# Optimization experiments

Measured on AMD Instinct MI355X. Metric: run time of the kernel, lower is better.

Reference implementation:

```python
import jax, jax.numpy as jnp
import numpy as np

B, LP, LQ, H = 16, 2048, 2048, 1024

def setup_inputs() -> dict:
    key = jax.random.key(0)
    k1, k2, k3 = jax.random.split(key, 3)
    proj_p = jax.random.normal(k1, (B, LP, H), dtype=jnp.float32)
    proj_q = jax.random.normal(k2, (B, LQ, H), dtype=jnp.float32)
    # nn.Linear(hidden_size, hidden_size): W stored as [out, in], y = x @ W.T + b
    W = jax.random.normal(k3, (H, H), dtype=jnp.float32) * (1.0 / np.sqrt(H))
    b = jnp.zeros((H,), dtype=jnp.float32)
    return {"proj_p": proj_p, "proj_q": proj_q, "W": W, "b": b}

def reference(proj_p, proj_q, W, b):
    # trans_q = Linear(proj_q)
    trans_q = jnp.einsum('bqh,oh->bqo', proj_q, W) + b            # [B,LQ,H]
    # UNscaled attention scores: proj_p @ trans_q^T
    att_weights = jnp.einsum('bph,bqh->bpq', proj_p, trans_q)     # [B,LP,LQ]
    att_norm = jax.nn.softmax(att_weights, axis=-1)
    att_vec = jnp.einsum('bpq,bqh->bph', att_norm, proj_q)        # [B,LP,H]
    # same linear weight reused, then ReLU
    out = jax.nn.relu(jnp.einsum('bph,oh->bpo', att_vec, W) + b)
    return out
```

## Files before the change

kernel.cpp:

```cpp
#include <hip/hip_runtime.h>

typedef _Float16 f16;
typedef _Float16 f16x8 __attribute__((ext_vector_type(8)));
typedef _Float16 f16x4 __attribute__((ext_vector_type(4)));
typedef float    f32x16 __attribute__((ext_vector_type(16)));

#define GLDS(gp, lp) __builtin_amdgcn_global_load_lds( \
    (const __attribute__((address_space(1))) void*)(gp), \
    (__attribute__((address_space(3))) void*)(lp), 16, 0, 0)

template<typename OUT_T, bool BIAS, bool RELU>
__global__ __launch_bounds__(512, 2)
void gemm_bt2(const f16* __restrict__ A, const f16* __restrict__ Bm,
              OUT_T* __restrict__ C, const float* __restrict__ bias,
              int M, int N, int K, long sA, long sB, long sC)
{
    constexpr int TSZ = 256 * 64;
    __shared__ alignas(16) f16 As[2 * TSZ];
    __shared__ alignas(16) f16 Bs[2 * TSZ];

    int bx = blockIdx.x, by = blockIdx.y;
    {
        const int gx = gridDim.x;
        const int l = by * gx + bx;
        const int W = gx * 8;
        const int ygrp = l / W;
        const int rem = l - ygrp * W;
        bx = rem >> 3;
        by = ygrp * 8 + (rem & 7);
    }
    const int z = blockIdx.z;
    A  += (long)z * sA;
    Bm += (long)z * sB;
    C  += (long)z * sC;

    const int tid  = threadIdx.x;
    const int wid  = tid >> 6;
    const int lane = tid & 63;
    const int lr = lane & 31;
    const int lh = lane >> 5;
    const int m0 = by * 256;
    const int n0 = bx * 256;
    const int wm = (wid >> 2) * 128;
    const int wn = (wid & 3) * 64;

    const int sr = tid >> 3;
    const int sg = ((tid & 7) ^ (sr & 7)) * 8;
    const f16* agS = A  + (long)(m0 + sr) * K + sg;
    const f16* bgS = Bm + (long)(n0 + sr) * K + sg;
    f16* aD = As + wid * (8 * 64);
    f16* bD = Bs + wid * (8 * 64);

    const int s7  = lr & 7;
    const int xs0 = ((0 + lh) ^ s7) * 8;
    const int xs1 = ((2 + lh) ^ s7) * 8;
    const int xs2 = ((4 + lh) ^ s7) * 8;
    const int xs3 = ((6 + lh) ^ s7) * 8;
    const f16* aR = As + (wm + lr) * 64;
    const f16* bR = Bs + (wn + lr) * 64;

    f32x16 acc[4][2];
#pragma unroll
    for (int mi = 0; mi < 4; ++mi)
#pragma unroll
        for (int ni = 0; ni < 2; ++ni)
#pragma unroll
            for (int r = 0; r < 16; ++r) acc[mi][ni][r] = 0.f;

    f16x8 b00, b01, b02, b03, b10, b11, b12, b13;

    const int NT = K >> 6;

#define GAc(buf, R0, kt) GLDS(agS + (long)(R0) * K + (kt), aD + (buf) * TSZ + (R0) * 64)
#define GBc(buf, R0, kt) GLDS(bgS + (long)(R0) * K + (kt), bD + (buf) * TSZ + (R0) * 64)

    GBc(0,   0, 0);  GBc(0,  64, 0);  GBc(0, 128, 0);  GBc(0, 192, 0);
    GAc(0,   0, 0);  GAc(0,  64, 0);  GAc(0, 128, 0);  GAc(0, 192, 0);
    GBc(1,   0, 64); GBc(1,  64, 64); GBc(1, 128, 64); GBc(1, 192, 64);
    GAc(1,   0, 64); GAc(1, 128, 64);
    asm volatile("s_waitcnt vmcnt(6)" ::: "memory");
    __builtin_amdgcn_s_barrier();

#define MFMA8(mi) \
    acc[mi][0] = __builtin_amdgcn_mfma_f32_32x32x16_f16(af0, b00, acc[mi][0], 0, 0, 0); \
    acc[mi][1] = __builtin_amdgcn_mfma_f32_32x32x16_f16(af0, b10, acc[mi][1], 0, 0, 0); \
    acc[mi][0] = __builtin_amdgcn_mfma_f32_32x32x16_f16(af1, b01, acc[mi][0], 0, 0, 0); \
    acc[mi][1] = __builtin_amdgcn_mfma_f32_32x32x16_f16(af1, b11, acc[mi][1], 0, 0, 0); \
    acc[mi][0] = __builtin_amdgcn_mfma_f32_32x32x16_f16(af2, b02, acc[mi][0], 0, 0, 0); \
    acc[mi][1] = __builtin_amdgcn_mfma_f32_32x32x16_f16(af2, b12, acc[mi][1], 0, 0, 0); \
    acc[mi][0] = __builtin_amdgcn_mfma_f32_32x32x16_f16(af3, b03, acc[mi][0], 0, 0, 0); \
    acc[mi][1] = __builtin_amdgcn_mfma_f32_32x32x16_f16(af3, b13, acc[mi][1], 0, 0, 0);

#define PH(buf, mi, VW, ...) { \
    if ((mi) == 0) { \
        b00 = *(const f16x8*)(bR + (buf) * TSZ + xs0); \
        b01 = *(const f16x8*)(bR + (buf) * TSZ + xs1); \
        b02 = *(const f16x8*)(bR + (buf) * TSZ + xs2); \
        b03 = *(const f16x8*)(bR + (buf) * TSZ + xs3); \
        b10 = *(const f16x8*)(bR + (buf) * TSZ + 2048 + xs0); \
        b11 = *(const f16x8*)(bR + (buf) * TSZ + 2048 + xs1); \
        b12 = *(const f16x8*)(bR + (buf) * TSZ + 2048 + xs2); \
        b13 = *(const f16x8*)(bR + (buf) * TSZ + 2048 + xs3); \
    } \
    f16x8 af0 = *(const f16x8*)(aR + (buf) * TSZ + (mi) * 2048 + xs0); \
    f16x8 af1 = *(const f16x8*)(aR + (buf) * TSZ + (mi) * 2048 + xs1); \
    f16x8 af2 = *(const f16x8*)(aR + (buf) * TSZ + (mi) * 2048 + xs2); \
    f16x8 af3 = *(const f16x8*)(aR + (buf) * TSZ + (mi) * 2048 + xs3); \
    __VA_ARGS__ \
    __builtin_amdgcn_s_barrier(); \
    asm volatile("s_waitcnt lgkmcnt(0)" ::: "memory"); \
    __builtin_amdgcn_s_setprio(1); \
    MFMA8(mi) \
    __builtin_amdgcn_s_setprio(0); \
    if (VW) { asm volatile("s_waitcnt vmcnt(6)" ::: "memory"); } \
    __builtin_amdgcn_s_barrier(); \
}

    for (int i = 0; i < NT / 2; ++i) {
        const long k1 = (long)(2 * i + 1) << 6;
        const long kA = (2 * i + 2 < NT) ? ((long)(2 * i + 2) << 6) : 0;
        const long kB = (2 * i + 3 < NT) ? ((long)(2 * i + 3) << 6) : 0;
        PH(0, 0, 0, GAc(1,  64, k1); GAc(1, 192, k1);)
        PH(0, 1, 0, GBc(0,   0, kA); GBc(0,  64, kA);)
        PH(0, 2, 0, GBc(0, 128, kA); GBc(0, 192, kA);)
        PH(0, 3, 1, GAc(0,   0, kA); GAc(0, 128, kA);)
        PH(1, 0, 0, GAc(0,  64, kA); GAc(0, 192, kA);)
        PH(1, 1, 0, GBc(1,   0, kB); GBc(1,  64, kB);)
        PH(1, 2, 0, GBc(1, 128, kB); GBc(1, 192, kB);)
        PH(1, 3, 1, GAc(1,   0, kB); GAc(1, 128, kB);)
    }

    asm volatile("s_waitcnt vmcnt(0)" ::: "memory");

#pragma unroll
    for (int ni = 0; ni < 2; ++ni) {
        const int gc = n0 + wn + ni * 32 + lr;
        const float bv = BIAS ? bias[gc] : 0.0f;
#pragma unroll
        for (int mi = 0; mi < 4; ++mi) {
#pragma unroll
            for (int r = 0; r < 16; ++r) {
                const int row = (r & 3) + 8 * (r >> 2) + 4 * lh;
                const int gr = m0 + wm + mi * 32 + row;
                float v = acc[mi][ni][r] + bv;
                if (RELU) v = fmaxf(v, 0.0f);
                C[(long)gr * N + gc] = (OUT_T)v;
            }
        }
    }
#undef PH
#undef MFMA8
#undef GAc
#undef GBc
}

template<typename OUT_T, bool BIAS, bool RELU>
__global__ __launch_bounds__(512, 2)
void gemm_bt3(const f16* __restrict__ A, const f16* __restrict__ Bm,
              OUT_T* __restrict__ C, const float* __restrict__ bias,
              int M, int N, int K, long sA, long sB, long sC)
{
    constexpr int TSA = 256 * 64;
    constexpr int TSB = 128 * 64;
    __shared__ alignas(16) f16 As[2 * TSA];
    __shared__ alignas(16) f16 Bs[2 * TSB];

    int bx = blockIdx.x, by = blockIdx.y;
    {
        const int gx = gridDim.x;
        const int l = by * gx + bx;
        const int W = gx * 8;
        const int ygrp = l / W;
        const int rem = l - ygrp * W;
        bx = rem >> 3;
        by = ygrp * 8 + (rem & 7);
    }
    const int z = blockIdx.z;
    A  += (long)z * sA;
    Bm += (long)z * sB;
    C  += (long)z * sC;

    const int tid  = threadIdx.x;
    const int wid  = tid >> 6;
    const int lane = tid & 63;
    const int lr = lane & 31;
    const int lh = lane >> 5;
    const int m0 = by * 256;
    const int n0 = bx * 128;
    const int wm = (wid >> 1) * 64;
    const int wn = (wid & 1) * 64;

    const int sr = tid >> 3;
    const int sg = ((tid & 7) ^ (sr & 7)) * 8;
    const f16* agS = A  + (long)(m0 + sr) * K + sg;
    const f16* bgS = Bm + (long)(n0 + sr) * K + sg;
    f16* aD = As + wid * (8 * 64);
    f16* bD = Bs + wid * (8 * 64);

    const int s7  = lr & 7;
    const int xs0 = ((0 + lh) ^ s7) * 8;
    const int xs1 = ((2 + lh) ^ s7) * 8;
    const int xs2 = ((4 + lh) ^ s7) * 8;
    const int xs3 = ((6 + lh) ^ s7) * 8;
    const f16* aR = As + (wm + lr) * 64;
    const f16* bR = Bs + (wn + lr) * 64;

    f32x16 acc[2][2];
#pragma unroll
    for (int mi = 0; mi < 2; ++mi)
#pragma unroll
        for (int ni = 0; ni < 2; ++ni)
#pragma unroll
            for (int r = 0; r < 16; ++r) acc[mi][ni][r] = 0.f;

    f16x8 b00, b01, b02, b03, b10, b11, b12, b13;

    const int NT = K >> 6;

#define GA3(buf, R0, kt) GLDS(agS + (long)(R0) * K + (kt), aD + (buf) * TSA + (R0) * 64)
#define GB3(buf, R0, kt) GLDS(bgS + (long)(R0) * K + (kt), bD + (buf) * TSB + (R0) * 64)

    GB3(0,   0, 0);  GB3(0,  64, 0);
    GA3(0,   0, 0);  GA3(0,  64, 0);  GA3(0, 128, 0);  GA3(0, 192, 0);
    GB3(1,   0, 64); GB3(1,  64, 64);
    asm volatile("s_waitcnt vmcnt(2)" ::: "memory");
    __builtin_amdgcn_s_barrier();

#define MFMA8_3(mi) \
    acc[mi][0] = __builtin_amdgcn_mfma_f32_32x32x16_f16(af0, b00, acc[mi][0], 0, 0, 0); \
    acc[mi][1] = __builtin_amdgcn_mfma_f32_32x32x16_f16(af0, b10, acc[mi][1], 0, 0, 0); \
    acc[mi][0] = __builtin_amdgcn_mfma_f32_32x32x16_f16(af1, b01, acc[mi][0], 0, 0, 0); \
    acc[mi][1] = __builtin_amdgcn_mfma_f32_32x32x16_f16(af1, b11, acc[mi][1], 0, 0, 0); \
    acc[mi][0] = __builtin_amdgcn_mfma_f32_32x32x16_f16(af2, b02, acc[mi][0], 0, 0, 0); \
    acc[mi][1] = __builtin_amdgcn_mfma_f32_32x32x16_f16(af2, b12, acc[mi][1], 0, 0, 0); \
    acc[mi][0] = __builtin_amdgcn_mfma_f32_32x32x16_f16(af3, b03, acc[mi][0], 0, 0, 0); \
    acc[mi][1] = __builtin_amdgcn_mfma_f32_32x32x16_f16(af3, b13, acc[mi][1], 0, 0, 0);

#define PH3(buf, mi, VW, ...) { \
    if ((mi) == 0) { \
        b00 = *(const f16x8*)(bR + (buf) * TSB + xs0); \
        b01 = *(const f16x8*)(bR + (buf) * TSB + xs1); \
        b02 = *(const f16x8*)(bR + (buf) * TSB + xs2); \
        b03 = *(const f16x8*)(bR + (buf) * TSB + xs3); \
        b10 = *(const f16x8*)(bR + (buf) * TSB + 2048 + xs0); \
        b11 = *(const f16x8*)(bR + (buf) * TSB + 2048 + xs1); \
        b12 = *(const f16x8*)(bR + (buf) * TSB + 2048 + xs2); \
        b13 = *(const f16x8*)(bR + (buf) * TSB + 2048 + xs3); \
    } \
    f16x8 af0 = *(const f16x8*)(aR + (buf) * TSA + (mi) * 2048 + xs0); \
    f16x8 af1 = *(const f16x8*)(aR + (buf) * TSA + (mi) * 2048 + xs1); \
    f16x8 af2 = *(const f16x8*)(aR + (buf) * TSA + (mi) * 2048 + xs2); \
    f16x8 af3 = *(const f16x8*)(aR + (buf) * TSA + (mi) * 2048 + xs3); \
    __VA_ARGS__ \
    __builtin_amdgcn_s_barrier(); \
    asm volatile("s_waitcnt lgkmcnt(0)" ::: "memory"); \
    __builtin_amdgcn_s_setprio(1); \
    MFMA8_3(mi) \
    __builtin_amdgcn_s_setprio(0); \
    if (VW) { asm volatile("s_waitcnt vmcnt(2)" ::: "memory"); } \
    __builtin_amdgcn_s_barrier(); \
}

    for (int i = 0; i < NT / 2; ++i) {
        const long k1 = (long)(2 * i + 1) << 6;
        const long kA = (2 * i + 2 < NT) ? ((long)(2 * i + 2) << 6) : 0;
        const long kB = (2 * i + 3 < NT) ? ((long)(2 * i + 3) << 6) : 0;
        PH3(0, 0, 0, GA3(1,   0, k1); GA3(1,  64, k1); GA3(1, 128, k1); GA3(1, 192, k1);)
        PH3(0, 1, 1, GB3(0,   0, kA); GB3(0,  64, kA);)
        PH3(1, 0, 0, GA3(0,   0, kA); GA3(0,  64, kA); GA3(0, 128, kA); GA3(0, 192, kA);)
        PH3(1, 1, 1, GB3(1,   0, kB); GB3(1,  64, kB);)
    }

    asm volatile("s_waitcnt vmcnt(0)" ::: "memory");

#pragma unroll
    for (int ni = 0; ni < 2; ++ni) {
        const int gc = n0 + wn + ni * 32 + lr;
        const float bv = BIAS ? bias[gc] : 0.0f;
#pragma unroll
        for (int mi = 0; mi < 2; ++mi) {
#pragma unroll
            for (int r = 0; r < 16; ++r) {
                const int row = (r & 3) + 8 * (r >> 2) + 4 * lh;
                const int gr = m0 + wm + mi * 32 + row;
                float v = acc[mi][ni][r] + bv;
                if (RELU) v = fmaxf(v, 0.0f);
                C[(long)gr * N + gc] = (OUT_T)v;
            }
        }
    }
#undef PH3
#undef MFMA8_3
#undef GA3
#undef GB3
}

__global__ __launch_bounds__(256)
void cast_f32_f16(const float* __restrict__ X, f16* __restrict__ Y)
{
    const long i = ((long)blockIdx.x * 256 + threadIdx.x) * 8;
    float4 a = *(const float4*)(X + i);
    float4 b = *(const float4*)(X + i + 4);
    f16x8 h = {(f16)a.x, (f16)a.y, (f16)a.z, (f16)a.w,
               (f16)b.x, (f16)b.y, (f16)b.z, (f16)b.w};
    *(f16x8*)(Y + i) = h;
}

__global__ __launch_bounds__(256)
void cast_q_dual(const float* __restrict__ X, f16* __restrict__ Yrow,
                 f16* __restrict__ Ytr)
{
    __shared__ f16 t[64][72];
    const float* Xb = X + (long)blockIdx.z * (2048L * 1024);
    f16* Yrb = Yrow + (long)blockIdx.z * (2048L * 1024);
    f16* Ytb = Ytr  + (long)blockIdx.z * (1024L * 2048);
    const int r0 = blockIdx.y * 64;
    const int c0 = blockIdx.x * 64;
    const int tid = threadIdx.x;
    const int tr = tid >> 4;
    const int tc = (tid & 15) * 4;
#pragma unroll
    for (int rr = 0; rr < 64; rr += 16) {
        float4 v = *(const float4*)(Xb + (long)(r0 + tr + rr) * 1024 + c0 + tc);
        f16x4 h = {(f16)v.x, (f16)v.y, (f16)v.z, (f16)v.w};
        *(f16x4*)&t[tr + rr][tc] = h;
        *(f16x4*)(Yrb + (long)(r0 + tr + rr) * 1024 + c0 + tc) = h;
    }
    __syncthreads();
#pragma unroll
    for (int rr = 0; rr < 64; rr += 16) {
        const int orow = tr + rr;
        f16x4 o = {t[tc + 0][orow], t[tc + 1][orow], t[tc + 2][orow], t[tc + 3][orow]};
        *(f16x4*)(Ytb + (long)(c0 + orow) * 2048 + r0 + tc) = o;
    }
}

__global__ __launch_bounds__(256)
void softmax_p(const float* __restrict__ S, f16* __restrict__ P)
{
    const long row = blockIdx.x;
    const float* s = S + row * 2048;
    f16* p = P + row * 2048;
    const int tid = threadIdx.x;
    const int wid = tid >> 6, lane = tid & 63;

    float4 a = *(const float4*)(s + tid * 8);
    float4 b = *(const float4*)(s + tid * 8 + 4);
    float v[8] = {a.x, a.y, a.z, a.w, b.x, b.y, b.z, b.w};

    float m = v[0];
#pragma unroll
    for (int j = 1; j < 8; ++j) m = fmaxf(m, v[j]);
#pragma unroll
    for (int off = 32; off > 0; off >>= 1) m = fmaxf(m, __shfl_xor(m, off, 64));

    __shared__ float red[8];
    if (lane == 0) red[wid] = m;
    __syncthreads();
    m = fmaxf(fmaxf(red[0], red[1]), fmaxf(red[2], red[3]));

    float sum = 0.f;
#pragma unroll
    for (int j = 0; j < 8; ++j) { v[j] = __expf(v[j] - m); sum += v[j]; }
#pragma unroll
    for (int off = 32; off > 0; off >>= 1) sum += __shfl_xor(sum, off, 64);
    if (lane == 0) red[4 + wid] = sum;
    __syncthreads();
    sum = red[4] + red[5] + red[6] + red[7];

    const float inv = 1.0f / sum;
    f16x8 h = {(f16)(v[0] * inv), (f16)(v[1] * inv), (f16)(v[2] * inv), (f16)(v[3] * inv),
               (f16)(v[4] * inv), (f16)(v[5] * inv), (f16)(v[6] * inv), (f16)(v[7] * inv)};
    *(f16x8*)(p + tid * 8) = h;
}

extern "C" void kernel_launch(void* const* d_in, const int* in_sizes, int n_in,
                              void* d_out, int out_size, void* d_ws, size_t ws_size,
                              hipStream_t stream)
{
    const float* proj_p = (const float*)d_in[0];
    const float* proj_q = (const float*)d_in[1];
    const float* W      = (const float*)d_in[2];
    const float* bias   = (const float*)d_in[3];
    float* out = (float*)d_out;

    constexpr long Bc = 16, L = 2048, H = 1024, NB = 4;
    constexpr long nPQ = Bc * L * H;

    char* ws = (char*)d_ws;
    f16*   pB  = (f16*)(ws + 0L);
    f16*   qB  = (f16*)(ws + 67108864L);
    f16*   qBt = (f16*)(ws + 134217728L);
    f16*   tQ  = (f16*)(ws + 201326592L);
    f16*   aV  = (f16*)(ws + 268435456L);
    f16*   Wb  = (f16*)(ws + 335544320L);
    float* S   = (float*)(ws + 337641472L);
    f16*   P   = (f16*)(ws + 404750336L);

    cast_f32_f16<<<nPQ / (256 * 8), 256, 0, stream>>>(proj_p, pB);
    cast_f32_f16<<<(H * H) / (256 * 8), 256, 0, stream>>>(W, Wb);
    cast_q_dual<<<dim3(16, 32, 16), 256, 0, stream>>>(proj_q, qB, qBt);

    gemm_bt2<f16, true, false><<<dim3(H / 256, (Bc * L) / 256, 1), 512, 0, stream>>>(
        qB, Wb, tQ, bias, (int)(Bc * L), (int)H, (int)H, 0, 0, 0);

    for (int c = 0; c < 4; ++c) {
        const long boff = (long)c * NB * L * H;
        gemm_bt2<float, false, false><<<dim3(L / 256, L / 256, NB), 512, 0, stream>>>(
            pB + boff, tQ + boff, S, nullptr, (int)L, (int)L, (int)H,
            L * H, L * H, L * L);
        softmax_p<<<NB * L, 256, 0, stream>>>(S, P);
        gemm_bt3<f16, false, false><<<dim3(H / 128, L / 256, NB), 512, 0, stream>>>(
            P, qBt + (long)c * NB * H * L, aV + boff, nullptr, (int)L, (int)H, (int)L,
            L * L, H * L, L * H);
    }

    gemm_bt2<float, false, true><<<dim3(H / 256, (Bc * L) / 256, 1), 512, 0, stream>>>(
        aV, Wb, out, bias, (int)(Bc * L), (int)H, (int)H, 0, 0, 0);
}
```

Measured before the change: 968.3 us.

## Load B operand directly from global into registers, bypassing LDS

Both GEMM kernels now stop staging the B tile in shared memory. Each wave loads its own B fragments straight from global memory into registers, issuing one tile ahead, and the vmcnt waits are adjusted to match. This removes the LDS traffic, LDS capacity and barrier coupling for B, which could improve occupancy. In exchange, B data that several waves of a block share is fetched redundantly through L2/L1, and the global-load latency must be hidden by register prefetching, which raises register pressure.

```diff
diff --git a/kernel.cpp b/kernel.cpp
--- a/kernel.cpp
+++ b/kernel.cpp
@@ -17,7 +17,6 @@
 {
     constexpr int TSZ = 256 * 64;
     __shared__ alignas(16) f16 As[2 * TSZ];
-    __shared__ alignas(16) f16 Bs[2 * TSZ];
 
     int bx = blockIdx.x, by = blockIdx.y;
     {
@@ -46,10 +45,8 @@
 
     const int sr = tid >> 3;
     const int sg = ((tid & 7) ^ (sr & 7)) * 8;
-    const f16* agS = A  + (long)(m0 + sr) * K + sg;
-    const f16* bgS = Bm + (long)(n0 + sr) * K + sg;
+    const f16* agS = A + (long)(m0 + sr) * K + sg;
     f16* aD = As + wid * (8 * 64);
-    f16* bD = Bs + wid * (8 * 64);
 
     const int s7  = lr & 7;
     const int xs0 = ((0 + lh) ^ s7) * 8;
@@ -57,7 +54,9 @@
     const int xs2 = ((4 + lh) ^ s7) * 8;
     const int xs3 = ((6 + lh) ^ s7) * 8;
     const f16* aR = As + (wm + lr) * 64;
-    const f16* bR = Bs + (wn + lr) * 64;
+
+    const f16* bgl0 = Bm + (long)(n0 + wn + lr) * K + lh * 8;
+    const f16* bgl1 = bgl0 + (long)32 * K;
 
     f32x16 acc[4][2];
 #pragma unroll
@@ -67,41 +66,34 @@
 #pragma unroll
             for (int r = 0; r < 16; ++r) acc[mi][ni][r] = 0.f;
 
-    f16x8 b00, b01, b02, b03, b10, b11, b12, b13;
+    f16x8 bb0, bb1, bb2, bb3, bb4, bb5, bb6, bb7;
 
     const int NT = K >> 6;
 
 #define GAc(buf, R0, kt) GLDS(agS + (long)(R0) * K + (kt), aD + (buf) * TSZ + (R0) * 64)
-#define GBc(buf, R0, kt) GLDS(bgS + (long)(R0) * K + (kt), bD + (buf) * TSZ + (R0) * 64)
-
-    GBc(0,   0, 0);  GBc(0,  64, 0);  GBc(0, 128, 0);  GBc(0, 192, 0);
+#define BLD(kt) __builtin_amdgcn_sched_barrier(0); \
+    bb0 = *(const f16x8*)(bgl0 + (kt));      bb1 = *(const f16x8*)(bgl0 + (kt) + 16); \
+    bb2 = *(const f16x8*)(bgl0 + (kt) + 32); bb3 = *(const f16x8*)(bgl0 + (kt) + 48); \
+    bb4 = *(const f16x8*)(bgl1 + (kt));      bb5 = *(const f16x8*)(bgl1 + (kt) + 16); \
+    bb6 = *(const f16x8*)(bgl1 + (kt) + 32); bb7 = *(const f16x8*)(bgl1 + (kt) + 48);
+
+    BLD(0)
     GAc(0,   0, 0);  GAc(0,  64, 0);  GAc(0, 128, 0);  GAc(0, 192, 0);
-    GBc(1,   0, 64); GBc(1,  64, 64); GBc(1, 128, 64); GBc(1, 192, 64);
     GAc(1,   0, 64); GAc(1, 128, 64);
-    asm volatile("s_waitcnt vmcnt(6)" ::: "memory");
+    asm volatile("s_waitcnt vmcnt(2)" ::: "memory");
     __builtin_amdgcn_s_barrier();
 
 #define MFMA8(mi) \
-    acc[mi][0] = __builtin_amdgcn_mfma_f32_32x32x16_f16(af0, b00, acc[mi][0], 0, 0, 0); \
-    acc[mi][1] = __builtin_amdgcn_mfma_f32_32x32x16_f16(af0, b10, acc[mi][1], 0, 0, 0); \
-    acc[mi][0] = __builtin_amdgcn_mfma_f32_32x32x16_f16(af1, b01, acc[mi][0], 0, 0, 0); \
-    acc[mi][1] = __builtin_amdgcn_mfma_f32_32x32x16_f16(af1, b11, acc[mi][1], 0, 0, 0); \
-    acc[mi][0] = __builtin_amdgcn_mfma_f32_32x32x16_f16(af2, b02, acc[mi][0], 0, 0, 0); \
-    acc[mi][1] = __builtin_amdgcn_mfma_f32_32x32x16_f16(af2, b12, acc[mi][1], 0, 0, 0); \
-    acc[mi][0] = __builtin_amdgcn_mfma_f32_32x32x16_f16(af3, b03, acc[mi][0], 0, 0, 0); \
-    acc[mi][1] = __builtin_amdgcn_mfma_f32_32x32x16_f16(af3, b13, acc[mi][1], 0, 0, 0);
-
-#define PH(buf, mi, VW, ...) { \
-    if ((mi) == 0) { \
-        b00 = *(const f16x8*)(bR + (buf) * TSZ + xs0); \
-        b01 = *(const f16x8*)(bR + (buf) * TSZ + xs1); \
-        b02 = *(const f16x8*)(bR + (buf) * TSZ + xs2); \
-        b03 = *(const f16x8*)(bR + (buf) * TSZ + xs3); \
-        b10 = *(const f16x8*)(bR + (buf) * TSZ + 2048 + xs0); \
-        b11 = *(const f16x8*)(bR + (buf) * TSZ + 2048 + xs1); \
-        b12 = *(const f16x8*)(bR + (buf) * TSZ + 2048 + xs2); \
-        b13 = *(const f16x8*)(bR + (buf) * TSZ + 2048 + xs3); \
-    } \
+    acc[mi][0] = __builtin_amdgcn_mfma_f32_32x32x16_f16(af0, bb0, acc[mi][0], 0, 0, 0); \
+    acc[mi][1] = __builtin_amdgcn_mfma_f32_32x32x16_f16(af0, bb4, acc[mi][1], 0, 0, 0); \
+    acc[mi][0] = __builtin_amdgcn_mfma_f32_32x32x16_f16(af1, bb1, acc[mi][0], 0, 0, 0); \
+    acc[mi][1] = __builtin_amdgcn_mfma_f32_32x32x16_f16(af1, bb5, acc[mi][1], 0, 0, 0); \
+    acc[mi][0] = __builtin_amdgcn_mfma_f32_32x32x16_f16(af2, bb2, acc[mi][0], 0, 0, 0); \
+    acc[mi][1] = __builtin_amdgcn_mfma_f32_32x32x16_f16(af2, bb6, acc[mi][1], 0, 0, 0); \
+    acc[mi][0] = __builtin_amdgcn_mfma_f32_32x32x16_f16(af3, bb3, acc[mi][0], 0, 0, 0); \
+    acc[mi][1] = __builtin_amdgcn_mfma_f32_32x32x16_f16(af3, bb7, acc[mi][1], 0, 0, 0);
+
+#define PH(buf, mi, VW, BL, ...) { \
     f16x8 af0 = *(const f16x8*)(aR + (buf) * TSZ + (mi) * 2048 + xs0); \
     f16x8 af1 = *(const f16x8*)(aR + (buf) * TSZ + (mi) * 2048 + xs1); \
     f16x8 af2 = *(const f16x8*)(aR + (buf) * TSZ + (mi) * 2048 + xs2); \
@@ -112,7 +104,8 @@
     __builtin_amdgcn_s_setprio(1); \
     MFMA8(mi) \
     __builtin_amdgcn_s_setprio(0); \
-    if (VW) { asm volatile("s_waitcnt vmcnt(6)" ::: "memory"); } \
+    BL \
+    if (VW) { asm volatile("s_waitcnt vmcnt(10)" ::: "memory"); } \
     __builtin_amdgcn_s_barrier(); \
 }
 
@@ -120,14 +113,14 @@
         const long k1 = (long)(2 * i + 1) << 6;
         const long kA = (2 * i + 2 < NT) ? ((long)(2 * i + 2) << 6) : 0;
         const long kB = (2 * i + 3 < NT) ? ((long)(2 * i + 3) << 6) : 0;
-        PH(0, 0, 0, GAc(1,  64, k1); GAc(1, 192, k1);)
-        PH(0, 1, 0, GBc(0,   0, kA); GBc(0,  64, kA);)
-        PH(0, 2, 0, GBc(0, 128, kA); GBc(0, 192, kA);)
-        PH(0, 3, 1, GAc(0,   0, kA); GAc(0, 128, kA);)
-        PH(1, 0, 0, GAc(0,  64, kA); GAc(0, 192, kA);)
-        PH(1, 1, 0, GBc(1,   0, kB); GBc(1,  64, kB);)
-        PH(1, 2, 0, GBc(1, 128, kB); GBc(1, 192, kB);)
-        PH(1, 3, 1, GAc(1,   0, kB); GAc(1, 128, kB);)
+        PH(0, 0, 0, ,        GAc(1,  64, k1); GAc(1, 192, k1);)
+        PH(0, 1, 0, ,        )
+        PH(0, 2, 0, ,        )
+        PH(0, 3, 1, BLD(k1), GAc(0,   0, kA); GAc(0, 128, kA);)
+        PH(1, 0, 0, ,        GAc(0,  64, kA); GAc(0, 192, kA);)
+        PH(1, 1, 0, ,        )
+        PH(1, 2, 0, ,        )
+        PH(1, 3, 1, BLD(kA), GAc(1,   0, kB); GAc(1, 128, kB);)
     }
 
     asm volatile("s_waitcnt vmcnt(0)" ::: "memory");
@@ -150,8 +143,8 @@
     }
 #undef PH
 #undef MFMA8
+#undef BLD
 #undef GAc
-#undef GBc
 }
 
 template<typename OUT_T, bool BIAS, bool RELU>
@@ -161,9 +154,7 @@
               int M, int N, int K, long sA, long sB, long sC)
 {
     constexpr int TSA = 256 * 64;
-    constexpr int TSB = 128 * 64;
     __shared__ alignas(16) f16 As[2 * TSA];
-    __shared__ alignas(16) f16 Bs[2 * TSB];
 
     int bx = blockIdx.x, by = blockIdx.y;
     {
@@ -192,10 +183,8 @@
 
     const int sr = tid >> 3;
     const int sg = ((tid & 7) ^ (sr & 7)) * 8;
-    const f16* agS = A  + (long)(m0 + sr) * K + sg;
-    const f16* bgS = Bm + (long)(n0 + sr) * K + sg;
+    const f16* agS = A + (long)(m0 + sr) * K + sg;
     f16* aD = As + wid * (8 * 64);
-    f16* bD = Bs + wid * (8 * 64);
 
     const int s7  = lr & 7;
     const int xs0 = ((0 + lh) ^ s7) * 8;
@@ -203,7 +192,9 @@
     const int xs2 = ((4 + lh) ^ s7) * 8;
     const int xs3 = ((6 + lh) ^ s7) * 8;
     const f16* aR = As + (wm + lr) * 64;
-    const f16* bR = Bs + (wn + lr) * 64;
+
+    const f16* bgl0 = Bm + (long)(n0 + wn + lr) * K + lh * 8;
+    const f16* bgl1 = bgl0 + (long)32 * K;
 
     f32x16 acc[2][2];
 #pragma unroll
@@ -213,40 +204,33 @@
 #pragma unroll
             for (int r = 0; r < 16; ++r) acc[mi][ni][r] = 0.f;
 
-    f16x8 b00, b01, b02, b03, b10, b11, b12, b13;
+    f16x8 bb0, bb1, bb2, bb3, bb4, bb5, bb6, bb7;
 
     const int NT = K >> 6;
 
 #define GA3(buf, R0, kt) GLDS(agS + (long)(R0) * K + (kt), aD + (buf) * TSA + (R0) * 64)
-#define GB3(buf, R0, kt) GLDS(bgS + (long)(R0) * K + (kt), bD + (buf) * TSB + (R0) * 64)
-
-    GB3(0,   0, 0);  GB3(0,  64, 0);
+#define BLD3(kt) __builtin_amdgcn_sched_barrier(0); \
+    bb0 = *(const f16x8*)(bgl0 + (kt));      bb1 = *(const f16x8*)(bgl0 + (kt) + 16); \
+    bb2 = *(const f16x8*)(bgl0 + (kt) + 32); bb3 = *(const f16x8*)(bgl0 + (kt) + 48); \
+    bb4 = *(const f16x8*)(bgl1 + (kt));      bb5 = *(const f16x8*)(bgl1 + (kt) + 16); \
+    bb6 = *(const f16x8*)(bgl1 + (kt) + 32); bb7 = *(const f16x8*)(bgl1 + (kt) + 48);
+
+    BLD3(0)
     GA3(0,   0, 0);  GA3(0,  64, 0);  GA3(0, 128, 0);  GA3(0, 192, 0);
-    GB3(1,   0, 64); GB3(1,  64, 64);
-    asm volatile("s_waitcnt vmcnt(2)" ::: "memory");
+    asm volatile("s_waitcnt vmcnt(0)" ::: "memory");
     __builtin_amdgcn_s_barrier();
 
 #define MFMA8_3(mi) \
-    acc[mi][0] = __builtin_amdgcn_mfma_f32_32x32x16_f16(af0, b00, acc[mi][0], 0, 0, 0); \
-    acc[mi][1] = __builtin_amdgcn_mfma_f32_32x32x16_f16(af0, b10, acc[mi][1], 0, 0, 0); \
-    acc[mi][0] = __builtin_amdgcn_mfma_f32_32x32x16_f16(af1, b01, acc[mi][0], 0, 0, 0); \
-    acc[mi][1] = __builtin_amdgcn_mfma_f32_32x32x16_f16(af1, b11, acc[mi][1], 0, 0, 0); \
-    acc[mi][0] = __builtin_amdgcn_mfma_f32_32x32x16_f16(af2, b02, acc[mi][0], 0, 0, 0); \
-    acc[mi][1] = __builtin_amdgcn_mfma_f32_32x32x16_f16(af2, b12, acc[mi][1], 0, 0, 0); \
-    acc[mi][0] = __builtin_amdgcn_mfma_f32_32x32x16_f16(af3, b03, acc[mi][0], 0, 0, 0); \
-    acc[mi][1] = __builtin_amdgcn_mfma_f32_32x32x16_f16(af3, b13, acc[mi][1], 0, 0, 0);
-
-#define PH3(buf, mi, VW, ...) { \
-    if ((mi) == 0) { \
-        b00 = *(const f16x8*)(bR + (buf) * TSB + xs0); \
-        b01 = *(const f16x8*)(bR + (buf) * TSB + xs1); \
-        b02 = *(const f16x8*)(bR + (buf) * TSB + xs2); \
-        b03 = *(const f16x8*)(bR + (buf) * TSB + xs3); \
-        b10 = *(const f16x8*)(bR + (buf) * TSB + 2048 + xs0); \
-        b11 = *(const f16x8*)(bR + (buf) * TSB + 2048 + xs1); \
-        b12 = *(const f16x8*)(bR + (buf) * TSB + 2048 + xs2); \
-        b13 = *(const f16x8*)(bR + (buf) * TSB + 2048 + xs3); \
-    } \
+    acc[mi][0] = __builtin_amdgcn_mfma_f32_32x32x16_f16(af0, bb0, acc[mi][0], 0, 0, 0); \
+    acc[mi][1] = __builtin_amdgcn_mfma_f32_32x32x16_f16(af0, bb4, acc[mi][1], 0, 0, 0); \
+    acc[mi][0] = __builtin_amdgcn_mfma_f32_32x32x16_f16(af1, bb1, acc[mi][0], 0, 0, 0); \
+    acc[mi][1] = __builtin_amdgcn_mfma_f32_32x32x16_f16(af1, bb5, acc[mi][1], 0, 0, 0); \
+    acc[mi][0] = __builtin_amdgcn_mfma_f32_32x32x16_f16(af2, bb2, acc[mi][0], 0, 0, 0); \
+    acc[mi][1] = __builtin_amdgcn_mfma_f32_32x32x16_f16(af2, bb6, acc[mi][1], 0, 0, 0); \
+    acc[mi][0] = __builtin_amdgcn_mfma_f32_32x32x16_f16(af3, bb3, acc[mi][0], 0, 0, 0); \
+    acc[mi][1] = __builtin_amdgcn_mfma_f32_32x32x16_f16(af3, bb7, acc[mi][1], 0, 0, 0);
+
+#define PH3(buf, mi, VW, BL, ...) { \
     f16x8 af0 = *(const f16x8*)(aR + (buf) * TSA + (mi) * 2048 + xs0); \
     f16x8 af1 = *(const f16x8*)(aR + (buf) * TSA + (mi) * 2048 + xs1); \
     f16x8 af2 = *(const f16x8*)(aR + (buf) * TSA + (mi) * 2048 + xs2); \
@@ -257,18 +241,18 @@
     __builtin_amdgcn_s_setprio(1); \
     MFMA8_3(mi) \
     __builtin_amdgcn_s_setprio(0); \
-    if (VW) { asm volatile("s_waitcnt vmcnt(2)" ::: "memory"); } \
+    BL \
+    if (VW) { asm volatile("s_waitcnt vmcnt(8)" ::: "memory"); } \
     __builtin_amdgcn_s_barrier(); \
 }
 
     for (int i = 0; i < NT / 2; ++i) {
         const long k1 = (long)(2 * i + 1) << 6;
         const long kA = (2 * i + 2 < NT) ? ((long)(2 * i + 2) << 6) : 0;
-        const long kB = (2 * i + 3 < NT) ? ((long)(2 * i + 3) << 6) : 0;
-        PH3(0, 0, 0, GA3(1,   0, k1); GA3(1,  64, k1); GA3(1, 128, k1); GA3(1, 192, k1);)
-        PH3(0, 1, 1, GB3(0,   0, kA); GB3(0,  64, kA);)
-        PH3(1, 0, 0, GA3(0,   0, kA); GA3(0,  64, kA); GA3(0, 128, kA); GA3(0, 192, kA);)
-        PH3(1, 1, 1, GB3(1,   0, kB); GB3(1,  64, kB);)
+        PH3(0, 0, 0, ,         GA3(1, 0, k1); GA3(1, 64, k1); GA3(1, 128, k1); GA3(1, 192, k1);)
+        PH3(0, 1, 1, BLD3(k1), )
+        PH3(1, 0, 0, ,         GA3(0, 0, kA); GA3(0, 64, kA); GA3(0, 128, kA); GA3(0, 192, kA);)
+        PH3(1, 1, 1, BLD3(kA), )
     }
 
     asm volatile("s_waitcnt vmcnt(0)" ::: "memory");
@@ -291,8 +275,8 @@
     }
 #undef PH3
 #undef MFMA8_3
+#undef BLD3
 #undef GA3
-#undef GB3
 }
 
 __global__ __launch_bounds__(256)
```

Result: slower. 1.325 ms (+36.8%).

## Load B operand directly from global into registers, dropping B LDS staging

Applied to the files above, without the earlier changes.

In gemm_bt2 the B tile is no longer staged through shared memory. Each wave loads its own 64 B-rows straight from global memory into two register sets that alternate as a double buffer, and the vmcnt waits are adjusted to match. This cuts LDS footprint and LDS read/write traffic for B, which could allow higher occupancy. The cost is redundant global loads of B across the waves that share columns, plus more vector registers, with a risk of register pressure or spilling.

```diff
diff --git a/kernel.cpp b/kernel.cpp
--- a/kernel.cpp
+++ b/kernel.cpp
@@ -17,7 +17,6 @@
 {
     constexpr int TSZ = 256 * 64;
     __shared__ alignas(16) f16 As[2 * TSZ];
-    __shared__ alignas(16) f16 Bs[2 * TSZ];
 
     int bx = blockIdx.x, by = blockIdx.y;
     {
@@ -46,10 +45,8 @@
 
     const int sr = tid >> 3;
     const int sg = ((tid & 7) ^ (sr & 7)) * 8;
-    const f16* agS = A  + (long)(m0 + sr) * K + sg;
-    const f16* bgS = Bm + (long)(n0 + sr) * K + sg;
+    const f16* agS = A + (long)(m0 + sr) * K + sg;
     f16* aD = As + wid * (8 * 64);
-    f16* bD = Bs + wid * (8 * 64);
 
     const int s7  = lr & 7;
     const int xs0 = ((0 + lh) ^ s7) * 8;
@@ -57,7 +54,9 @@
     const int xs2 = ((4 + lh) ^ s7) * 8;
     const int xs3 = ((6 + lh) ^ s7) * 8;
     const f16* aR = As + (wm + lr) * 64;
-    const f16* bR = Bs + (wn + lr) * 64;
+
+    const f16* bgl0 = Bm + (long)(n0 + wn + lr) * K + lh * 8;
+    const f16* bgl1 = bgl0 + (long)32 * K;
 
     f32x16 acc[4][2];
 #pragma unroll
@@ -67,41 +66,36 @@
 #pragma unroll
             for (int r = 0; r < 16; ++r) acc[mi][ni][r] = 0.f;
 
-    f16x8 b00, b01, b02, b03, b10, b11, b12, b13;
+    f16x8 bx0, bx1, bx2, bx3, bx4, bx5, bx6, bx7;
+    f16x8 by0, by1, by2, by3, by4, by5, by6, by7;
 
     const int NT = K >> 6;
 
 #define GAc(buf, R0, kt) GLDS(agS + (long)(R0) * K + (kt), aD + (buf) * TSZ + (R0) * 64)
-#define GBc(buf, R0, kt) GLDS(bgS + (long)(R0) * K + (kt), bD + (buf) * TSZ + (R0) * 64)
-
-    GBc(0,   0, 0);  GBc(0,  64, 0);  GBc(0, 128, 0);  GBc(0, 192, 0);
+#define BLDS(S, kt) __builtin_amdgcn_sched_barrier(0); \
+    S##0 = *(const f16x8*)(bgl0 + (kt));      S##1 = *(const f16x8*)(bgl0 + (kt) + 16); \
+    S##2 = *(const f16x8*)(bgl0 + (kt) + 32); S##3 = *(const f16x8*)(bgl0 + (kt) + 48); \
+    S##4 = *(const f16x8*)(bgl1 + (kt));      S##5 = *(const f16x8*)(bgl1 + (kt) + 16); \
+    S##6 = *(const f16x8*)(bgl1 + (kt) + 32); S##7 = *(const f16x8*)(bgl1 + (kt) + 48);
+
+    BLDS(bx, 0)
     GAc(0,   0, 0);  GAc(0,  64, 0);  GAc(0, 128, 0);  GAc(0, 192, 0);
-    GBc(1,   0, 64); GBc(1,  64, 64); GBc(1, 128, 64); GBc(1, 192, 64);
     GAc(1,   0, 64); GAc(1, 128, 64);
-    asm volatile("s_waitcnt vmcnt(6)" ::: "memory");
+    BLDS(by, 64)
+    asm volatile("s_waitcnt vmcnt(10)" ::: "memory");
     __builtin_amdgcn_s_barrier();
 
-#define MFMA8(mi) \
-    acc[mi][0] = __builtin_amdgcn_mfma_f32_32x32x16_f16(af0, b00, acc[mi][0], 0, 0, 0); \
-    acc[mi][1] = __builtin_amdgcn_mfma_f32_32x32x16_f16(af0, b10, acc[mi][1], 0, 0, 0); \
-    acc[mi][0] = __builtin_amdgcn_mfma_f32_32x32x16_f16(af1, b01, acc[mi][0], 0, 0, 0); \
-    acc[mi][1] = __builtin_amdgcn_mfma_f32_32x32x16_f16(af1, b11, acc[mi][1], 0, 0, 0); \
-    acc[mi][0] = __builtin_amdgcn_mfma_f32_32x32x16_f16(af2, b02, acc[mi][0], 0, 0, 0); \
-    acc[mi][1] = __builtin_amdgcn_mfma_f32_32x32x16_f16(af2, b12, acc[mi][1], 0, 0, 0); \
-    acc[mi][0] = __builtin_amdgcn_mfma_f32_32x32x16_f16(af3, b03, acc[mi][0], 0, 0, 0); \
-    acc[mi][1] = __builtin_amdgcn_mfma_f32_32x32x16_f16(af3, b13, acc[mi][1], 0, 0, 0);
-
-#define PH(buf, mi, VW, ...) { \
-    if ((mi) == 0) { \
-        b00 = *(const f16x8*)(bR + (buf) * TSZ + xs0); \
-        b01 = *(const f16x8*)(bR + (buf) * TSZ + xs1); \
-        b02 = *(const f16x8*)(bR + (buf) * TSZ + xs2); \
-        b03 = *(const f16x8*)(bR + (buf) * TSZ + xs3); \
-        b10 = *(const f16x8*)(bR + (buf) * TSZ + 2048 + xs0); \
-        b11 = *(const f16x8*)(bR + (buf) * TSZ + 2048 + xs1); \
-        b12 = *(const f16x8*)(bR + (buf) * TSZ + 2048 + xs2); \
-        b13 = *(const f16x8*)(bR + (buf) * TSZ + 2048 + xs3); \
-    } \
+#define MFMA8(mi, S) \
+    acc[mi][0] = __builtin_amdgcn_mfma_f32_32x32x16_f16(af0, S##0, acc[mi][0], 0, 0, 0); \
+    acc[mi][1] = __builtin_amdgcn_mfma_f32_32x32x16_f16(af0, S##4, acc[mi][1], 0, 0, 0); \
+    acc[mi][0] = __builtin_amdgcn_mfma_f32_32x32x16_f16(af1, S##1, acc[mi][0], 0, 0, 0); \
+    acc[mi][1] = __builtin_amdgcn_mfma_f32_32x32x16_f16(af1, S##5, acc[mi][1], 0, 0, 0); \
+    acc[mi][0] = __builtin_amdgcn_mfma_f32_32x32x16_f16(af2, S##2, acc[mi][0], 0, 0, 0); \
+    acc[mi][1] = __builtin_amdgcn_mfma_f32_32x32x16_f16(af2, S##6, acc[mi][1], 0, 0, 0); \
+    acc[mi][0] = __builtin_amdgcn_mfma_f32_32x32x16_f16(af3, S##3, acc[mi][0], 0, 0, 0); \
+    acc[mi][1] = __builtin_amdgcn_mfma_f32_32x32x16_f16(af3, S##7, acc[mi][1], 0, 0, 0);
+
+#define PH(buf, mi, S, VW, BL, ...) { \
     f16x8 af0 = *(const f16x8*)(aR + (buf) * TSZ + (mi) * 2048 + xs0); \
     f16x8 af1 = *(const f16x8*)(aR + (buf) * TSZ + (mi) * 2048 + xs1); \
     f16x8 af2 = *(const f16x8*)(aR + (buf) * TSZ + (mi) * 2048 + xs2); \
@@ -110,9 +104,10 @@
     __builtin_amdgcn_s_barrier(); \
     asm volatile("s_waitcnt lgkmcnt(0)" ::: "memory"); \
     __builtin_amdgcn_s_setprio(1); \
-    MFMA8(mi) \
+    MFMA8(mi, S) \
     __builtin_amdgcn_s_setprio(0); \
-    if (VW) { asm volatile("s_waitcnt vmcnt(6)" ::: "memory"); } \
+    BL \
+    if (VW) { asm volatile("s_waitcnt vmcnt(10)" ::: "memory"); } \
     __builtin_amdgcn_s_barrier(); \
 }
 
@@ -120,14 +115,14 @@
         const long k1 = (long)(2 * i + 1) << 6;
         const long kA = (2 * i + 2 < NT) ? ((long)(2 * i + 2) << 6) : 0;
         const long kB = (2 * i + 3 < NT) ? ((long)(2 * i + 3) << 6) : 0;
-        PH(0, 0, 0, GAc(1,  64, k1); GAc(1, 192, k1);)
-        PH(0, 1, 0, GBc(0,   0, kA); GBc(0,  64, kA);)
-        PH(0, 2, 0, GBc(0, 128, kA); GBc(0, 192, kA);)
-        PH(0, 3, 1, GAc(0,   0, kA); GAc(0, 128, kA);)
-        PH(1, 0, 0, GAc(0,  64, kA); GAc(0, 192, kA);)
-        PH(1, 1, 0, GBc(1,   0, kB); GBc(1,  64, kB);)
-        PH(1, 2, 0, GBc(1, 128, kB); GBc(1, 192, kB);)
-        PH(1, 3, 1, GAc(1,   0, kB); GAc(1, 128, kB);)
+        PH(0, 0, bx, 0, ,             GAc(1,  64, k1); GAc(1, 192, k1);)
+        PH(0, 1, bx, 0, ,             )
+        PH(0, 2, bx, 0, ,             )
+        PH(0, 3, bx, 1, BLDS(bx, kA), GAc(0,   0, kA); GAc(0, 128, kA);)
+        PH(1, 0, by, 0, ,             GAc(0,  64, kA); GAc(0, 192, kA);)
+        PH(1, 1, by, 0, ,             )
+        PH(1, 2, by, 0, ,             )
+        PH(1, 3, by, 1, BLDS(by, kB), GAc(1,   0, kB); GAc(1, 128, kB);)
     }
 
     asm volatile("s_waitcnt vmcnt(0)" ::: "memory");
@@ -150,8 +145,8 @@
     }
 #undef PH
 #undef MFMA8
+#undef BLDS
 #undef GAc
-#undef GBc
 }
 
 template<typename OUT_T, bool BIAS, bool RELU>
```

Result: slower. 1.100 ms (+13.6%).
